# Kernel optimization log

Measured on AMD Instinct MI355X. Metric: run time of the kernel, lower is better.

Reference implementation:

```python
import jax, jax.numpy as jnp
import numpy as np

N, L, D = 8192, 50, 64          # batch nodes, history length, embed_dim
NUM_ITEMS, NUM_ATTRS, NUM_FAM = 50000, 100000, 100000


def setup_inputs() -> dict:
    key = jax.random.key(0)
    ks = jax.random.split(key, 12)
    scale = 0.05
    return {
        "nodes": jax.random.randint(ks[0], (N,), 0, NUM_ITEMS),
        "history_va": jax.random.randint(ks[1], (N, L), 0, NUM_ATTRS),
        "history_af": jax.random.randint(ks[2], (N, L), 0, NUM_FAM),
        "v2e_w": jax.random.normal(ks[3], (NUM_ITEMS, D), jnp.float32) * scale,
        "a2e_w": jax.random.normal(ks[4], (NUM_ATTRS, D), jnp.float32) * scale,
        "f2e_w": jax.random.normal(ks[5], (NUM_FAM, D), jnp.float32) * scale,
        "W1": jax.random.normal(ks[6], (3 * D, D), jnp.float32) * scale,
        "b1": jnp.zeros((D,), jnp.float32),
        "W2": jax.random.normal(ks[7], (D, D), jnp.float32) * scale,
        "b2": jnp.zeros((D,), jnp.float32),
        "w3": jax.random.normal(ks[8], (D, 1), jnp.float32) * scale,
        "b3": jnp.zeros((1,), jnp.float32),
    }


def reference(nodes, history_va, history_af, v2e_w, a2e_w, f2e_w,
              W1, b1, W2, b2, w3, b3):
    # Batched form of the per-node loop (va=True branch).
    e_va = a2e_w[history_va]                       # [N, L, D] gathered attr embeds
    e_af = f2e_w[history_af]                       # [N, L, D] gathered famous embeds
    va_rep = v2e_w[nodes]                          # [N, D]    target item embed
    rep = jnp.broadcast_to(va_rep[:, None, :], e_va.shape)
    x = jnp.concatenate([e_va, rep, e_af], axis=-1)  # [N, L, 3D]
    h = jax.nn.relu(x @ W1 + b1)                   # [N, L, D]
    h = jax.nn.relu(h @ W2 + b2)                   # [N, L, D]
    scores = (h @ w3 + b3)[..., 0]                 # [N, L]
    att = jax.nn.softmax(scores, axis=1)           # softmax over history dim
    # e_va.T @ att per node  ==  weighted sum over history
    return jnp.einsum("nld,nl->nd", e_va, att)     # [N, D]
```

## Files before the change

### kernel.cpp

```cpp
#include <hip/hip_runtime.h>
#include <hip/hip_bf16.h>

typedef __bf16 bf16x8 __attribute__((ext_vector_type(8)));
typedef __bf16 bf16x4 __attribute__((ext_vector_type(4)));
typedef float  f32x4  __attribute__((ext_vector_type(4)));

#define HL   50
#define DD   64
#define NPB  2
#define MR   112
#define MT   7
#define XSS  136
#define RSS  72

__global__ __launch_bounds__(256, 4) void va_agg_kernel(
    const int*   __restrict__ nodes,
    const int*   __restrict__ hva,
    const int*   __restrict__ haf,
    const float* __restrict__ v2e,
    const float* __restrict__ a2e,
    const float* __restrict__ f2e,
    const float* __restrict__ W1,
    const float* __restrict__ b1,
    const float* __restrict__ W2,
    const float* __restrict__ b2,
    const float* __restrict__ w3,
    float*       __restrict__ out)
{
    __shared__ __bf16 xs[MR * XSS];
    __shared__ __bf16 reps[16 * RSS];
    __shared__ float  rbias_s[NPB * DD];
    __shared__ float  pbuf[4 * MR];
    __shared__ float  att_s[NPB * DD];

    const int tid  = threadIdx.x;
    const int w    = tid >> 6;
    const int lane = tid & 63;
    const int lq   = lane & 15;
    const int quad = lane >> 4;
    const int col  = w * 16 + lq;
    const int n0   = blockIdx.x * NPB;

    bf16x8 b1f[4], b1u[2], b2f[2];
    #pragma unroll
    for (int t = 0; t < 4; ++t)
        #pragma unroll
        for (int j = 0; j < 8; ++j) {
            int keff = t * 32 + quad * 8 + j;
            int krow = (keff < 64) ? keff : keff + 64;
            b1f[t][j] = (__bf16)W1[krow * 64 + col];
        }
    #pragma unroll
    for (int t = 0; t < 2; ++t)
        #pragma unroll
        for (int j = 0; j < 8; ++j) {
            b1u[t][j] = (__bf16)W1[(64 + t * 32 + quad * 8 + j) * 64 + col];
            b2f[t][j] = (__bf16)W2[(t * 32 + quad * 8 + j) * 64 + col];
        }
    const float w3c = w3[col];
    const float b1c = b1[col];
    const float b2c = b2[col];

    {
        bf16x4 z = {(__bf16)0.f, (__bf16)0.f, (__bf16)0.f, (__bf16)0.f};
        for (int i = tid; i < (MR - NPB * HL) * 32; i += 256) {
            int r = NPB * HL + (i >> 5);
            int c = (i & 31) * 4;
            *(bf16x4*)&xs[r * XSS + c] = z;
        }
        for (int i = tid; i < 14 * 16; i += 256) {
            int r = 2 + (i >> 4);
            int q = i & 15;
            *(bf16x4*)&reps[r * RSS + q * 4] = z;
        }
        if (tid < NPB * 16) {
            int n = tid >> 4, q = tid & 15;
            int nd = nodes[n0 + n];
            float4 v = *(const float4*)(v2e + (size_t)nd * DD + q * 4);
            bf16x4 pk = {(__bf16)v.x, (__bf16)v.y, (__bf16)v.z, (__bf16)v.w};
            *(bf16x4*)&reps[n * RSS + q * 4] = pk;
        }
    }
    __syncthreads();

    {
        const int* hb = hva + n0 * HL;
        const int* fb = haf + n0 * HL;
        #pragma unroll
        for (int i = 0; i < 13; ++i) {
            int t = i * 256 + tid;
            if (t < NPB * HL * 2 * 16) {
                int r = t >> 4, q = t & 15;
                bool va = (r < NPB * HL);
                int gr = va ? r : r - NPB * HL;
                int idx = va ? hb[gr] : fb[gr];
                const float* src = (va ? a2e : f2e) + (size_t)idx * DD + q * 4;
                float4 v = *(const float4*)src;
                bf16x4 pk = {(__bf16)v.x, (__bf16)v.y, (__bf16)v.z, (__bf16)v.w};
                *(bf16x4*)&xs[gr * XSS + (va ? 0 : DD) + q * 4] = pk;
            }
        }
        f32x4 rb = {0.f, 0.f, 0.f, 0.f};
        #pragma unroll
        for (int t = 0; t < 2; ++t) {
            bf16x8 a = *(const bf16x8*)&reps[lq * RSS + t * 32 + quad * 8];
            rb = __builtin_amdgcn_mfma_f32_16x16x32_bf16(a, b1u[t], rb, 0, 0, 0);
        }
        if (quad == 0) {
            rbias_s[0 * DD + col] = rb[0] + b1c;
            rbias_s[1 * DD + col] = rb[1] + b1c;
        }
    }
    __syncthreads();

    f32x4 acc[MT];
    #pragma unroll
    for (int mt = 0; mt < MT; ++mt)
        #pragma unroll
        for (int r = 0; r < 4; ++r) {
            int gr = mt * 16 + quad * 4 + r;
            acc[mt][r] = rbias_s[((gr >= HL) ? 1 : 0) * DD + col];
        }
    #pragma unroll
    for (int t = 0; t < 4; ++t)
        #pragma unroll
        for (int mt = 0; mt < MT; ++mt) {
            bf16x8 a = *(const bf16x8*)&xs[(mt * 16 + lq) * XSS + t * 32 + quad * 8];
            acc[mt] = __builtin_amdgcn_mfma_f32_16x16x32_bf16(a, b1f[t], acc[mt], 0, 0, 0);
        }
    __syncthreads();
    #pragma unroll
    for (int mt = 0; mt < MT; ++mt)
        #pragma unroll
        for (int r = 0; r < 4; ++r) {
            int gr = mt * 16 + quad * 4 + r;
            xs[gr * XSS + DD + col] = (__bf16)fmaxf(acc[mt][r], 0.f);
        }
    __syncthreads();

    f32x4 a2[MT];
    #pragma unroll
    for (int mt = 0; mt < MT; ++mt) a2[mt] = (f32x4){b2c, b2c, b2c, b2c};
    #pragma unroll
    for (int t = 0; t < 2; ++t)
        #pragma unroll
        for (int mt = 0; mt < MT; ++mt) {
            bf16x8 a = *(const bf16x8*)&xs[(mt * 16 + lq) * XSS + DD + t * 32 + quad * 8];
            a2[mt] = __builtin_amdgcn_mfma_f32_16x16x32_bf16(a, b2f[t], a2[mt], 0, 0, 0);
        }
    #pragma unroll
    for (int mt = 0; mt < MT; ++mt) {
        float p0 = fmaxf(a2[mt][0], 0.f) * w3c;
        float p1 = fmaxf(a2[mt][1], 0.f) * w3c;
        float p2 = fmaxf(a2[mt][2], 0.f) * w3c;
        float p3 = fmaxf(a2[mt][3], 0.f) * w3c;
        #pragma unroll
        for (int m = 1; m < 16; m <<= 1) {
            p0 += __shfl_xor(p0, m);
            p1 += __shfl_xor(p1, m);
            p2 += __shfl_xor(p2, m);
            p3 += __shfl_xor(p3, m);
        }
        if (lq == 0) {
            int rowb = mt * 16 + quad * 4;
            pbuf[w * MR + rowb + 0] = p0;
            pbuf[w * MR + rowb + 1] = p1;
            pbuf[w * MR + rowb + 2] = p2;
            pbuf[w * MR + rowb + 3] = p3;
        }
    }
    __syncthreads();

    if (w < NPB) {
        float s = -3.0e38f;
        if (lane < HL) {
            int gr = w * HL + lane;
            s = pbuf[gr] + pbuf[MR + gr] + pbuf[2 * MR + gr] + pbuf[3 * MR + gr];
        }
        float mx = s;
        #pragma unroll
        for (int m = 1; m < 64; m <<= 1) mx = fmaxf(mx, __shfl_xor(mx, m));
        float e = (lane < HL) ? __expf(s - mx) : 0.f;
        float sm = e;
        #pragma unroll
        for (int m = 1; m < 64; m <<= 1) sm += __shfl_xor(sm, m);
        att_s[w * DD + lane] = e / sm;
    }
    __syncthreads();

    {
        int n = w & 1, lh = w >> 1;
        float o0 = 0.f, o1 = 0.f;
        const int lb = lh * 25;
        #pragma unroll
        for (int i = 0; i < 25; i += 2) {
            int l = lb + i;
            o0 = fmaf(att_s[n * DD + l], (float)xs[(n * HL + l) * XSS + lane], o0);
            if (i + 1 < 25)
                o1 = fmaf(att_s[n * DD + l + 1], (float)xs[(n * HL + l + 1) * XSS + lane], o1);
        }
        pbuf[w * MR + lane] = o0 + o1;
    }
    __syncthreads();
    if (w < NPB) {
        float o = pbuf[w * MR + lane] + pbuf[(w + 2) * MR + lane];
        out[(size_t)(n0 + w) * DD + lane] = o;
    }
}

extern "C" void kernel_launch(void* const* d_in, const int* in_sizes, int n_in,
                              void* d_out, int out_size, void* d_ws, size_t ws_size,
                              hipStream_t stream) {
    const int*   nodes = (const int*)d_in[0];
    const int*   hva   = (const int*)d_in[1];
    const int*   haf   = (const int*)d_in[2];
    const float* v2e   = (const float*)d_in[3];
    const float* a2e   = (const float*)d_in[4];
    const float* f2e   = (const float*)d_in[5];
    const float* W1    = (const float*)d_in[6];
    const float* b1    = (const float*)d_in[7];
    const float* W2    = (const float*)d_in[8];
    const float* b2    = (const float*)d_in[9];
    const float* w3    = (const float*)d_in[10];
    float* out = (float*)d_out;

    const int N = in_sizes[0];
    const int blocks = N / NPB;
    va_agg_kernel<<<blocks, 256, 0, stream>>>(nodes, hva, haf, v2e, a2e, f2e,
                                              W1, b1, W2, b2, w3, out);
}
```

Measured before the change: 173.5 us.

## Drop shared staging buffers and barriers, keep rep bias and attention in registers

The target-item projection is now computed straight from registers loaded from v2e and broadcast with shuffles, so the reps and rbias shared arrays and one barrier go away. The zeroing of the padding rows is also removed. Every wave computes the softmax redundantly and broadcasts attention weights by shuffle, which drops another barrier and the att_s buffer. Partial outputs reuse the padding rows of xs, and the launch bound rises to 5 blocks per CU. The risk is extra register pressure, plus uninitialised padding rows, which only feed unused score rows.

```diff
diff --git a/kernel.cpp b/kernel.cpp
--- a/kernel.cpp
+++ b/kernel.cpp
@@ -11,9 +11,8 @@
 #define MR   112
 #define MT   7
 #define XSS  136
-#define RSS  72
-
-__global__ __launch_bounds__(256, 4) void va_agg_kernel(
+
+__global__ __launch_bounds__(256, 5) void va_agg_kernel(
     const int*   __restrict__ nodes,
     const int*   __restrict__ hva,
     const int*   __restrict__ haf,
@@ -28,10 +27,7 @@
     float*       __restrict__ out)
 {
     __shared__ __bf16 xs[MR * XSS];
-    __shared__ __bf16 reps[16 * RSS];
-    __shared__ float  rbias_s[NPB * DD];
     __shared__ float  pbuf[4 * MR];
-    __shared__ float  att_s[NPB * DD];
 
     const int tid  = threadIdx.x;
     const int w    = tid >> 6;
@@ -40,48 +36,6 @@
     const int quad = lane >> 4;
     const int col  = w * 16 + lq;
     const int n0   = blockIdx.x * NPB;
-
-    bf16x8 b1f[4], b1u[2], b2f[2];
-    #pragma unroll
-    for (int t = 0; t < 4; ++t)
-        #pragma unroll
-        for (int j = 0; j < 8; ++j) {
-            int keff = t * 32 + quad * 8 + j;
-            int krow = (keff < 64) ? keff : keff + 64;
-            b1f[t][j] = (__bf16)W1[krow * 64 + col];
-        }
-    #pragma unroll
-    for (int t = 0; t < 2; ++t)
-        #pragma unroll
-        for (int j = 0; j < 8; ++j) {
-            b1u[t][j] = (__bf16)W1[(64 + t * 32 + quad * 8 + j) * 64 + col];
-            b2f[t][j] = (__bf16)W2[(t * 32 + quad * 8 + j) * 64 + col];
-        }
-    const float w3c = w3[col];
-    const float b1c = b1[col];
-    const float b2c = b2[col];
-
-    {
-        bf16x4 z = {(__bf16)0.f, (__bf16)0.f, (__bf16)0.f, (__bf16)0.f};
-        for (int i = tid; i < (MR - NPB * HL) * 32; i += 256) {
-            int r = NPB * HL + (i >> 5);
-            int c = (i & 31) * 4;
-            *(bf16x4*)&xs[r * XSS + c] = z;
-        }
-        for (int i = tid; i < 14 * 16; i += 256) {
-            int r = 2 + (i >> 4);
-            int q = i & 15;
-            *(bf16x4*)&reps[r * RSS + q * 4] = z;
-        }
-        if (tid < NPB * 16) {
-            int n = tid >> 4, q = tid & 15;
-            int nd = nodes[n0 + n];
-            float4 v = *(const float4*)(v2e + (size_t)nd * DD + q * 4);
-            bf16x4 pk = {(__bf16)v.x, (__bf16)v.y, (__bf16)v.z, (__bf16)v.w};
-            *(bf16x4*)&reps[n * RSS + q * 4] = pk;
-        }
-    }
-    __syncthreads();
 
     {
         const int* hb = hva + n0 * HL;
@@ -100,17 +54,52 @@
                 *(bf16x4*)&xs[gr * XSS + (va ? 0 : DD) + q * 4] = pk;
             }
         }
-        f32x4 rb = {0.f, 0.f, 0.f, 0.f};
+    }
+
+    bf16x8 repf[2];
+    #pragma unroll
+    for (int t = 0; t < 2; ++t)
+        #pragma unroll
+        for (int j = 0; j < 8; ++j) repf[t][j] = (__bf16)0.f;
+    if (lq < NPB) {
+        int nd = nodes[n0 + lq];
+        const float* rp = v2e + (size_t)nd * DD;
         #pragma unroll
         for (int t = 0; t < 2; ++t) {
-            bf16x8 a = *(const bf16x8*)&reps[lq * RSS + t * 32 + quad * 8];
-            rb = __builtin_amdgcn_mfma_f32_16x16x32_bf16(a, b1u[t], rb, 0, 0, 0);
-        }
-        if (quad == 0) {
-            rbias_s[0 * DD + col] = rb[0] + b1c;
-            rbias_s[1 * DD + col] = rb[1] + b1c;
-        }
-    }
+            float4 v0 = *(const float4*)(rp + t * 32 + quad * 8);
+            float4 v1 = *(const float4*)(rp + t * 32 + quad * 8 + 4);
+            repf[t] = (bf16x8){(__bf16)v0.x, (__bf16)v0.y, (__bf16)v0.z, (__bf16)v0.w,
+                               (__bf16)v1.x, (__bf16)v1.y, (__bf16)v1.z, (__bf16)v1.w};
+        }
+    }
+
+    bf16x8 b1f[4], b1u[2], b2f[2];
+    #pragma unroll
+    for (int t = 0; t < 4; ++t)
+        #pragma unroll
+        for (int j = 0; j < 8; ++j) {
+            int keff = t * 32 + quad * 8 + j;
+            int krow = (keff < 64) ? keff : keff + 64;
+            b1f[t][j] = (__bf16)W1[krow * 64 + col];
+        }
+    #pragma unroll
+    for (int t = 0; t < 2; ++t)
+        #pragma unroll
+        for (int j = 0; j < 8; ++j) {
+            b1u[t][j] = (__bf16)W1[(64 + t * 32 + quad * 8 + j) * 64 + col];
+            b2f[t][j] = (__bf16)W2[(t * 32 + quad * 8 + j) * 64 + col];
+        }
+    const float w3c = w3[col];
+    const float b1c = b1[col];
+    const float b2c = b2[col];
+
+    f32x4 rb = {0.f, 0.f, 0.f, 0.f};
+    #pragma unroll
+    for (int t = 0; t < 2; ++t)
+        rb = __builtin_amdgcn_mfma_f32_16x16x32_bf16(repf[t], b1u[t], rb, 0, 0, 0);
+    const float bias0 = __shfl(rb[0], lq) + b1c;
+    const float bias1 = __shfl(rb[1], lq) + b1c;
+
     __syncthreads();
 
     f32x4 acc[MT];
@@ -119,7 +108,7 @@
         #pragma unroll
         for (int r = 0; r < 4; ++r) {
             int gr = mt * 16 + quad * 4 + r;
-            acc[mt][r] = rbias_s[((gr >= HL) ? 1 : 0) * DD + col];
+            acc[mt][r] = (gr >= HL) ? bias1 : bias0;
         }
     #pragma unroll
     for (int t = 0; t < 4; ++t)
@@ -171,10 +160,13 @@
     }
     __syncthreads();
 
-    if (w < NPB) {
+    const int n  = w & 1;
+    const int lh = w >> 1;
+    float att;
+    {
         float s = -3.0e38f;
         if (lane < HL) {
-            int gr = w * HL + lane;
+            int gr = n * HL + lane;
             s = pbuf[gr] + pbuf[MR + gr] + pbuf[2 * MR + gr] + pbuf[3 * MR + gr];
         }
         float mx = s;
@@ -184,27 +176,26 @@
         float sm = e;
         #pragma unroll
         for (int m = 1; m < 64; m <<= 1) sm += __shfl_xor(sm, m);
-        att_s[w * DD + lane] = e / sm;
-    }
-    __syncthreads();
+        att = e / sm;
+    }
 
     {
-        int n = w & 1, lh = w >> 1;
-        float o0 = 0.f, o1 = 0.f;
+        float o = 0.f;
         const int lb = lh * 25;
         #pragma unroll
-        for (int i = 0; i < 25; i += 2) {
+        for (int i = 0; i < 25; ++i) {
             int l = lb + i;
-            o0 = fmaf(att_s[n * DD + l], (float)xs[(n * HL + l) * XSS + lane], o0);
-            if (i + 1 < 25)
-                o1 = fmaf(att_s[n * DD + l + 1], (float)xs[(n * HL + l + 1) * XSS + lane], o1);
-        }
-        pbuf[w * MR + lane] = o0 + o1;
+            float av = __shfl(att, l);
+            o = fmaf(av, (float)xs[(n * HL + l) * XSS + lane], o);
+        }
+        float* op = (float*)&xs[(100 + w) * XSS + DD];
+        op[lane] = o;
     }
     __syncthreads();
     if (w < NPB) {
-        float o = pbuf[w * MR + lane] + pbuf[(w + 2) * MR + lane];
-        out[(size_t)(n0 + w) * DD + lane] = o;
+        const float* p0 = (const float*)&xs[(100 + w) * XSS + DD];
+        const float* p1 = (const float*)&xs[(100 + w + 2) * XSS + DD];
+        out[(size_t)(n0 + w) * DD + lane] = p0[lane] + p1[lane];
     }
 }
 
```

Result: no change. 174.4 us (+0.5%).
